# Performance work log

Hardware: AMD Instinct MI355X
Metric: run time of the kernel (lower is better)

The kernel has to match this reference:

```python
import jax, jax.numpy as jnp
import numpy as np

NUM_NODES = 200000
NUM_EDGES = 300000
NUM_QUERIES = 128
NUM_ENTITIES = 50000
N_DIMS = 256
N_DIMS_SM = 64
STATIC_DIM = 128
STATIC_SM = 32
G_IN = 2 * N_DIMS_SM + STATIC_SM + N_DIMS_SM  # 224


def leaky(x):
    return jnp.where(x > 0, x, 0.01 * x)


def setup_inputs() -> dict:
    key = jax.random.key(0)
    ks = jax.random.split(key, 24)
    W = 0.05  # weight scale to keep logits in a sane range
    inp = {
        'memorized_embedding': jax.random.normal(ks[0], (NUM_NODES, N_DIMS), jnp.float32),
        'node_score': jax.random.uniform(ks[1], (NUM_NODES,), jnp.float32),
        'rel_emb': jax.random.normal(ks[2], (NUM_EDGES, N_DIMS), jnp.float32),
        'query_src_ts_emb': jax.random.normal(ks[3], (NUM_QUERIES, STATIC_DIM), jnp.float32),
        'query_rel_emb': jax.random.normal(ks[4], (NUM_QUERIES, N_DIMS), jnp.float32),
        'eg_idx': jax.random.randint(ks[5], (NUM_EDGES,), 0, NUM_QUERIES, jnp.int32),
        'src_idx': jax.random.randint(ks[6], (NUM_EDGES,), 0, NUM_NODES, jnp.int32),
        'dst_idx': jax.random.randint(ks[7], (NUM_EDGES,), 0, NUM_NODES, jnp.int32),
        'entity_idx': jax.random.randint(ks[8], (NUM_NODES,), 0, NUM_ENTITIES, jnp.int32),
        'W_proj': W * jax.random.normal(ks[9], (N_DIMS, N_DIMS_SM), jnp.float32),
        'b_proj': W * jax.random.normal(ks[10], (N_DIMS_SM,), jnp.float32),
        'W_static': W * jax.random.normal(ks[11], (STATIC_DIM, STATIC_SM), jnp.float32),
        'b_static': W * jax.random.normal(ks[12], (STATIC_SM,), jnp.float32),
        'W_bs': W * jax.random.normal(ks[13], (N_DIMS, N_DIMS), jnp.float32),
        'b_bs': W * jax.random.normal(ks[14], (N_DIMS,), jnp.float32),
        'Wl': W * jax.random.normal(ks[15], (G_IN, N_DIMS_SM), jnp.float32),
        'bl': W * jax.random.normal(ks[16], (N_DIMS_SM,), jnp.float32),
        'Wr': W * jax.random.normal(ks[17], (G_IN, N_DIMS_SM), jnp.float32),
        'br': W * jax.random.normal(ks[18], (N_DIMS_SM,), jnp.float32),
        'Wc': W * jax.random.normal(ks[19], (N_DIMS_SM, N_DIMS_SM), jnp.float32),
        'bc': W * jax.random.normal(ks[20], (N_DIMS_SM,), jnp.float32),
    }
    return inp


def reference(memorized_embedding, node_score, rel_emb, query_src_ts_emb, query_rel_emb,
              eg_idx, src_idx, dst_idx, entity_idx,
              W_proj, b_proj, W_static, b_static, W_bs, b_bs,
              Wl, bl, Wr, br, Wc, bc):
    # one attention-flow step: linear_between_steps -> attention scoring (G) ->
    # per-source-node softmax -> attention propagation -> per-entity aggregation
    emb2 = leaky(memorized_embedding @ W_bs + b_bs)        # [N, d]
    # project all node embeddings once (linear commutes with gather)
    proj_all = emb2 @ W_proj + b_proj                       # [N, d_sm]
    hvi = proj_all[src_idx]                                 # [E, d_sm]
    hvj = proj_all[dst_idx]                                 # [E, d_sm]
    rel = rel_emb @ W_proj + b_proj                         # [E, d_sm]
    # context_dim_red
    qs = query_src_ts_emb @ W_static + b_static             # [B, static_sm]
    qr = query_rel_emb @ W_proj + b_proj                    # [B, d_sm]
    qs_e = qs[eg_idx]                                       # [E, static_sm]
    qr_e = qr[eg_idx]                                       # [E, d_sm]
    left = jnp.concatenate([hvi, rel, qs_e, qr_e], axis=-1)   # [E, G_IN]
    right = jnp.concatenate([hvj, rel, qs_e, qr_e], axis=-1)  # [E, G_IN]
    # G: sum(leaky(left W_l) * ((leaky(right W_r)) W_c))
    lh = leaky(left @ Wl + bl)                              # [E, d_sm]
    rh = leaky(right @ Wr + br) @ Wc + bc                   # [E, d_sm]
    logits = jnp.sum(lh * rh, axis=-1)                      # [E]
    # transition probability: softmax over outgoing edges of each source node
    seg_max = jax.ops.segment_max(logits, src_idx, num_segments=NUM_NODES)
    ex = jnp.exp(logits - seg_max[src_idx])
    denom = jax.ops.segment_sum(ex, src_idx, num_segments=NUM_NODES)
    trans = ex / denom[src_idx]
    # propagate node attention along edges (node_score_aggregation='sum')
    new_node_score = jax.ops.segment_sum(trans * node_score[src_idx], dst_idx,
                                         num_segments=NUM_NODES)
    # _aggregate_op_entity: sparse COO matmul == segment_sum over entity groups
    entity_att_score = jax.ops.segment_sum(new_node_score, entity_idx,
                                           num_segments=NUM_ENTITIES)
    return entity_att_score
```

## Files before the change

### kernel.cpp

```cpp
#include <hip/hip_runtime.h>
#include <hip/hip_bf16.h>

#define N_NODES 200000
#define N_EDGES 300000
#define N_Q     128
#define N_ENT   50000
#define D       256
#define DSM     64
#define SDIM    128
#define SSM     32

typedef __attribute__((ext_vector_type(8))) short bf16x8;
typedef __attribute__((ext_vector_type(4))) float f32x4;

__device__ __forceinline__ float leaky(float x){ return x > 0.f ? x : 0.01f*x; }

__device__ __forceinline__ unsigned short f2bf(float f){
  __hip_bfloat16 h = __float2bfloat16(f);
  return *reinterpret_cast<unsigned short*>(&h);
}
__device__ __forceinline__ unsigned pk2bf(float a, float b){
  float2 t; t.x = a; t.y = b;
  __hip_bfloat162 h = __float22bfloat162_rn(t);
  return *reinterpret_cast<unsigned*>(&h);
}
__device__ __forceinline__ float bf2f(unsigned short h){
  return __uint_as_float(((unsigned)h) << 16);
}

__device__ __forceinline__ void dev_pack(const float* __restrict__ src,
                                         unsigned short* __restrict__ dst,
                                         int K, int N, int id, int total){
  if (id >= total) return;
  int lane = id & 63, fb = id >> 6;
  int KB = K >> 5;
  int kb = fb % KB, nb = fb / KB;
  int k0 = kb*32 + ((lane>>4)<<3);
  int n  = nb*16 + (lane & 15);
  #pragma unroll
  for (int i = 0; i < 8; ++i) dst[(size_t)id*8 + i] = f2bf(src[(size_t)(k0+i)*N + n]);
}

__global__ void k_setup1(float* out, float* denom,
                         const float* __restrict__ Wp, const float* __restrict__ Wl,
                         const float* __restrict__ Wr, float* Wnlr, float* Wrlr,
                         const float* __restrict__ bp, float* cv,
                         const float* __restrict__ qsrc, const float* __restrict__ Ws,
                         const float* __restrict__ bs, const float* __restrict__ qrel,
                         float* qs, float* qr,
                         const float* __restrict__ Wbs, unsigned short* Wbs_pk,
                         const float* __restrict__ Wc, unsigned short* Wc_pk){
  int b = blockIdx.x, tid = threadIdx.x;
  if (b < 782){
    int id = b*256 + tid;
    if (id < N_ENT) out[id] = 0.f;
    if (id < N_NODES) denom[id] = 0.f;
  } else if (b < 1038){
    int id = (b-782)*256 + tid;
    int m = id >> 14, rem = id & 16383, k = rem >> 6, c = rem & 63;
    const float* Wsrc = (m & 1) ? Wr : Wl;
    int roff = (m >> 1) * 64;
    float s = 0.f;
    for (int i = 0; i < 64; ++i) s += Wp[k*64+i] * Wsrc[(roff+i)*64 + c];
    float* o = (m >> 1) ? Wrlr : Wnlr;
    o[k*128 + (m&1)*64 + c] = s;
  } else if (b == 1038){
    int m = tid >> 6, c = tid & 63;
    const float* Wsrc = (m & 1) ? Wr : Wl;
    int roff = (m >> 1) * 64;
    float s = 0.f;
    for (int i = 0; i < 64; ++i) s += bp[i] * Wsrc[(roff+i)*64 + c];
    cv[tid] = s;
  } else if (b < 1087){
    int id = (b-1039)*256 + tid;
    if (id < N_Q*SSM){
      int q = id >> 5, i = id & 31;
      float s = bs[i];
      for (int j = 0; j < SDIM; ++j) s += qsrc[q*SDIM+j] * Ws[j*SSM+i];
      qs[id] = s;
    } else {
      int id2 = id - N_Q*SSM;
      int q = id2 >> 6, i = id2 & 63;
      float s = bp[i];
      for (int j = 0; j < D; ++j) s += qrel[q*D+j] * Wp[j*DSM+i];
      qr[id2] = s;
    }
  } else if (b < 1119){
    dev_pack(Wbs, Wbs_pk, 256, 256, (b-1087)*256 + tid, 8192);
  } else {
    dev_pack(Wc, Wc_pk, 64, 64, (b-1119)*256 + tid, 512);
  }
}

__global__ void k_setup2(const float* __restrict__ qs, const float* __restrict__ qr,
                         const float* __restrict__ Wl, const float* __restrict__ bl,
                         const float* __restrict__ Wr, const float* __restrict__ br,
                         unsigned* qctx_p,
                         const float* __restrict__ Wnlr, unsigned short* Wn_pk,
                         const float* __restrict__ Wrlr, unsigned short* Wr_pk){
  int b = blockIdx.x, tid = threadIdx.x;
  if (b < 32){
    int id = b*256 + tid;
    int q = id >> 6, c = id & 63;
    float sl = bl[c], sr = br[c];
    for (int i = 0; i < SSM; ++i){
      float v = qs[q*SSM+i];
      sl += v * Wl[(128+i)*64+c];
      sr += v * Wr[(128+i)*64+c];
    }
    for (int i = 0; i < DSM; ++i){
      float v = qr[q*DSM+i];
      sl += v * Wl[(160+i)*64+c];
      sr += v * Wr[(160+i)*64+c];
    }
    qctx_p[id] = pk2bf(sl, sr);
  } else if (b < 48){
    dev_pack(Wnlr, Wn_pk, 256, 128, (b-32)*256 + tid, 4096);
  } else {
    dev_pack(Wrlr, Wr_pk, 256, 128, (b-48)*256 + tid, 4096);
  }
}

__global__ __launch_bounds__(256) void k_node(const float* __restrict__ A,
    const unsigned short* __restrict__ Wbs_pk, const float* __restrict__ bbs,
    const unsigned short* __restrict__ Wn_pk, const float* __restrict__ cv,
    unsigned short* __restrict__ node_l, unsigned short* __restrict__ node_r){
  __shared__ char smem[32768];
  int tid = threadIdx.x;
  int row0 = blockIdx.x * 64;
  {
    const float4* Ag = (const float4*)(A + (size_t)row0 * 256);
    #pragma unroll
    for (int it = 0; it < 16; ++it){
      int f = tid + 256*it;
      int r = f >> 6, c4 = f & 63;
      float4 v = Ag[f];
      uint2 u;
      u.x = pk2bf(v.x, v.y);
      u.y = pk2bf(v.z, v.w);
      int byte = (r << 9) + (c4 << 3);
      byte ^= (r & 7) << 4;
      *(uint2*)(smem + byte) = u;
    }
  }
  __syncthreads();
  int l = tid & 63, wn = tid >> 6;
  f32x4 acc[4][4];
  #pragma unroll
  for (int mf = 0; mf < 4; ++mf)
    #pragma unroll
    for (int nf = 0; nf < 4; ++nf) acc[mf][nf] = (f32x4){0.f,0.f,0.f,0.f};
  for (int kb = 0; kb < 8; ++kb){
    bf16x8 a[4], b[4];
    #pragma unroll
    for (int mf = 0; mf < 4; ++mf){
      int row = mf*16 + (l & 15);
      int byte = (row << 9) + kb*64 + ((l >> 4) << 4);
      byte ^= (row & 7) << 4;
      a[mf] = *(const bf16x8*)(smem + byte);
    }
    #pragma unroll
    for (int nf = 0; nf < 4; ++nf){
      int nb = wn*4 + nf;
      b[nf] = *(const bf16x8*)(Wbs_pk + ((size_t)(nb*8 + kb)*64 + l)*8);
    }
    #pragma unroll
    for (int mf = 0; mf < 4; ++mf)
      #pragma unroll
      for (int nf = 0; nf < 4; ++nf)
        acc[mf][nf] = __builtin_amdgcn_mfma_f32_16x16x32_bf16(a[mf], b[nf], acc[mf][nf], 0, 0, 0);
  }
  __syncthreads();
  #pragma unroll
  for (int mf = 0; mf < 4; ++mf)
    #pragma unroll
    for (int nf = 0; nf < 4; ++nf){
      int col = wn*64 + nf*16 + (l & 15);
      float bb = bbs[col];
      #pragma unroll
      for (int r = 0; r < 4; ++r){
        int row = mf*16 + ((l >> 4) << 2) + r;
        int byte = (row << 9) + col*2;
        byte ^= (row & 7) << 4;
        *(unsigned short*)(smem + byte) = f2bf(leaky(acc[mf][nf][r] + bb));
      }
    }
  __syncthreads();
  f32x4 acc2[4][2];
  #pragma unroll
  for (int mf = 0; mf < 4; ++mf){ acc2[mf][0] = (f32x4){0.f,0.f,0.f,0.f}; acc2[mf][1] = (f32x4){0.f,0.f,0.f,0.f}; }
  for (int kb = 0; kb < 8; ++kb){
    bf16x8 a[4], b[2];
    #pragma unroll
    for (int mf = 0; mf < 4; ++mf){
      int row = mf*16 + (l & 15);
      int byte = (row << 9) + kb*64 + ((l >> 4) << 4);
      byte ^= (row & 7) << 4;
      a[mf] = *(const bf16x8*)(smem + byte);
    }
    #pragma unroll
    for (int nf = 0; nf < 2; ++nf){
      int nb = wn*2 + nf;
      b[nf] = *(const bf16x8*)(Wn_pk + ((size_t)(nb*8 + kb)*64 + l)*8);
    }
    #pragma unroll
    for (int mf = 0; mf < 4; ++mf)
      #pragma unroll
      for (int nf = 0; nf < 2; ++nf)
        acc2[mf][nf] = __builtin_amdgcn_mfma_f32_16x16x32_bf16(a[mf], b[nf], acc2[mf][nf], 0, 0, 0);
  }
  #pragma unroll
  for (int mf = 0; mf < 4; ++mf)
    #pragma unroll
    for (int nf = 0; nf < 2; ++nf){
      int col = wn*32 + nf*16 + (l & 15);
      float cc = cv[col];
      #pragma unroll
      for (int r = 0; r < 4; ++r){
        int row = mf*16 + ((l >> 4) << 2) + r;
        unsigned short h = f2bf(acc2[mf][nf][r] + cc);
        size_t g = (size_t)(row0 + row);
        if (col < 64) node_l[g*64 + col] = h;
        else          node_r[g*64 + col - 64] = h;
      }
    }
}

__global__ __launch_bounds__(256) void k_edge(const float* __restrict__ relE,
    const unsigned short* __restrict__ Wr_pk, const unsigned short* __restrict__ Wc_pk,
    const float* __restrict__ cv, const float* __restrict__ bc,
    const unsigned short* __restrict__ node_l, const unsigned short* __restrict__ node_r,
    const unsigned* __restrict__ qctx_p,
    const int* __restrict__ src, const int* __restrict__ dst, const int* __restrict__ eg,
    float* __restrict__ exbuf, float* __restrict__ denom){
  __shared__ char smem[32768];
  unsigned short* sRL  = (unsigned short*)smem;
  char*           sLc  = smem + 16384;
  char*           sRin = smem + 24576;
  int tid = threadIdx.x;
  int e0 = blockIdx.x * 64;
  int l = tid & 63, wn = tid >> 6;

  int idxv;
  {
    int j = l & 15;
    int e = e0 + wn*16 + j;
    int ec = e < N_EDGES ? e : N_EDGES-1;
    const int* p = (l < 16) ? src : (l < 32) ? dst : eg;
    idxv = p[ec];
  }
  {
    const float4* Rg = (const float4*)relE;
    #pragma unroll
    for (int it = 0; it < 16; ++it){
      int f = tid + 256*it;
      int r = f >> 6, c4 = f & 63;
      int ge = e0 + r;
      float4 v = make_float4(0.f,0.f,0.f,0.f);
      if (ge < N_EDGES) v = Rg[(size_t)ge*64 + c4];
      uint2 u;
      u.x = pk2bf(v.x, v.y);
      u.y = pk2bf(v.z, v.w);
      int byte = (r << 9) + (c4 << 3);
      byte ^= (r & 7) << 4;
      *(uint2*)(smem + byte) = u;
    }
  }
  __syncthreads();

  f32x4 acc[4][2];
  #pragma unroll
  for (int mf = 0; mf < 4; ++mf){ acc[mf][0] = (f32x4){0.f,0.f,0.f,0.f}; acc[mf][1] = (f32x4){0.f,0.f,0.f,0.f}; }
  for (int kb = 0; kb < 8; ++kb){
    bf16x8 a[4], b[2];
    #pragma unroll
    for (int mf = 0; mf < 4; ++mf){
      int row = mf*16 + (l & 15);
      int byte = (row << 9) + kb*64 + ((l >> 4) << 4);
      byte ^= (row & 7) << 4;
      a[mf] = *(const bf16x8*)(smem + byte);
    }
    #pragma unroll
    for (int nf = 0; nf < 2; ++nf){
      int nb = wn*2 + nf;
      b[nf] = *(const bf16x8*)(Wr_pk + ((size_t)(nb*8 + kb)*64 + l)*8);
    }
    #pragma unroll
    for (int mf = 0; mf < 4; ++mf)
      #pragma unroll
      for (int nf = 0; nf < 2; ++nf)
        acc[mf][nf] = __builtin_amdgcn_mfma_f32_16x16x32_bf16(a[mf], b[nf], acc[mf][nf], 0, 0, 0);
  }
  __syncthreads();
  #pragma unroll
  for (int mf = 0; mf < 4; ++mf)
    #pragma unroll
    for (int nf = 0; nf < 2; ++nf){
      int col = wn*32 + nf*16 + (l & 15);
      float cc = cv[128 + col];
      #pragma unroll
      for (int r = 0; r < 4; ++r){
        int row = mf*16 + ((l >> 4) << 2) + r;
        int byte = (row << 8) + (col << 1);
        byte ^= (row & 12) << 3;
        *(unsigned short*)((char*)sRL + byte) = f2bf(acc[mf][nf][r] + cc);
      }
    }
  __syncthreads();
  #pragma unroll
  for (int j = 0; j < 16; ++j){
    int er = wn*16 + j;
    int e = e0 + er;
    int byteL = (er << 8) + (l << 1);      byteL ^= (er & 12) << 3;
    int byteR = (er << 8) + ((64+l) << 1); byteR ^= (er & 12) << 3;
    int bL = (er << 7) + (l << 1);         bL ^= (er & 12) << 3;
    int bR = (er << 7) + (l << 1);         bR ^= (er & 7) << 4;
    unsigned short lh16 = 0, rr16 = 0;
    if (e < N_EDGES){
      int s  = __shfl(idxv, j);
      int d2 = __shfl(idxv, 16 + j);
      int b  = __shfl(idxv, 32 + j);
      unsigned qv = qctx_p[b*64 + l];
      float lh = leaky(bf2f(node_l[(size_t)s*64 + l]) + bf2f(*(unsigned short*)((char*)sRL + byteL))
                       + bf2f((unsigned short)(qv & 0xFFFFu)));
      float rr = leaky(bf2f(node_r[(size_t)d2*64 + l]) + bf2f(*(unsigned short*)((char*)sRL + byteR))
                       + bf2f((unsigned short)(qv >> 16)));
      lh16 = f2bf(lh); rr16 = f2bf(rr);
    }
    *(unsigned short*)(sLc + bL) = lh16;
    *(unsigned short*)(sRin + bR) = rr16;
  }

  float bcv[4];
  #pragma unroll
  for (int nf = 0; nf < 4; ++nf) bcv[nf] = bc[nf*16 + (l & 15)];
  f32x4 acc2[4];
  #pragma unroll
  for (int nf = 0; nf < 4; ++nf) acc2[nf] = (f32x4){0.f,0.f,0.f,0.f};
  #pragma unroll
  for (int kb = 0; kb < 2; ++kb){
    int row = wn*16 + (l & 15);
    int byte = (row << 7) + kb*64 + ((l >> 4) << 4);
    byte ^= (row & 7) << 4;
    bf16x8 a = *(const bf16x8*)(sRin + byte);
    #pragma unroll
    for (int nf = 0; nf < 4; ++nf){
      bf16x8 bfr = *(const bf16x8*)(Wc_pk + ((size_t)(nf*2 + kb)*64 + l)*8);
      acc2[nf] = __builtin_amdgcn_mfma_f32_16x16x32_bf16(a, bfr, acc2[nf], 0, 0, 0);
    }
  }
  int srcj[4];
  float vr[4];
  #pragma unroll
  for (int r = 0; r < 4; ++r){
    int rowl = ((l >> 4) << 2) + r;
    srcj[r] = __shfl(idxv, rowl);
    int row = wn*16 + rowl;
    float v = 0.f;
    #pragma unroll
    for (int nf = 0; nf < 4; ++nf){
      int col = nf*16 + (l & 15);
      int byte = (row << 7) + (col << 1);
      byte ^= (row & 12) << 3;
      v += (acc2[nf][r] + bcv[nf]) * bf2f(*(unsigned short*)(sLc + byte));
    }
    v += __shfl_xor(v, 1); v += __shfl_xor(v, 2);
    v += __shfl_xor(v, 4); v += __shfl_xor(v, 8);
    vr[r] = v;
  }
  if ((l & 15) == 0){
    #pragma unroll
    for (int r = 0; r < 4; ++r){
      int rowl = ((l >> 4) << 2) + r;
      int e = e0 + wn*16 + rowl;
      if (e < N_EDGES){
        float ex = __expf(vr[r]);
        exbuf[e] = ex;
        atomicAdd(&denom[srcj[r]], ex);
      }
    }
  }
}

__global__ void k_passC(const float* __restrict__ exbuf, const float* __restrict__ denom,
                        const int* __restrict__ src, const int* __restrict__ dst,
                        const float* __restrict__ node_score, const int* __restrict__ ent,
                        float* __restrict__ out){
  int e = blockIdx.x*256 + threadIdx.x;
  if (e >= N_EDGES) return;
  int s = src[e];
  float tr = exbuf[e] / denom[s];
  atomicAdd(&out[ent[dst[e]]], tr * node_score[s]);
}

extern "C" void kernel_launch(void* const* d_in, const int* in_sizes, int n_in,
                              void* d_out, int out_size, void* d_ws, size_t ws_size,
                              hipStream_t stream){
  const float* mem   = (const float*)d_in[0];
  const float* nsc   = (const float*)d_in[1];
  const float* relE  = (const float*)d_in[2];
  const float* qsrc  = (const float*)d_in[3];
  const float* qrel  = (const float*)d_in[4];
  const int*   eg    = (const int*)d_in[5];
  const int*   src   = (const int*)d_in[6];
  const int*   dst   = (const int*)d_in[7];
  const int*   ent   = (const int*)d_in[8];
  const float* Wp    = (const float*)d_in[9];
  const float* bp    = (const float*)d_in[10];
  const float* Ws    = (const float*)d_in[11];
  const float* bs    = (const float*)d_in[12];
  const float* Wbs   = (const float*)d_in[13];
  const float* bbs   = (const float*)d_in[14];
  const float* Wl    = (const float*)d_in[15];
  const float* bl    = (const float*)d_in[16];
  const float* Wr    = (const float*)d_in[17];
  const float* br    = (const float*)d_in[18];
  const float* Wc    = (const float*)d_in[19];
  const float* bc    = (const float*)d_in[20];
  float* out = (float*)d_out;

  char* w = (char*)d_ws;
  auto alloc = [&](size_t bytes)->void*{
    void* p = (void*)w; w += (bytes + 255) & ~(size_t)255; return p;
  };
  float* Wnlr = (float*)alloc(32768*4);
  float* Wrlr = (float*)alloc(32768*4);
  unsigned short* Wbs_pk = (unsigned short*)alloc(65536*2);
  unsigned short* Wn_pk  = (unsigned short*)alloc(32768*2);
  unsigned short* Wr_pk  = (unsigned short*)alloc(32768*2);
  unsigned short* Wc_pk  = (unsigned short*)alloc(4096*2);
  float* cv  = (float*)alloc(256*4);
  float* qs  = (float*)alloc((size_t)N_Q*SSM*4);
  float* qr  = (float*)alloc((size_t)N_Q*DSM*4);
  unsigned* qctx_p = (unsigned*)alloc((size_t)N_Q*DSM*4);
  unsigned short* node_l = (unsigned short*)alloc((size_t)N_NODES*64*2);
  unsigned short* node_r = (unsigned short*)alloc((size_t)N_NODES*64*2);
  float* exbuf  = (float*)alloc((size_t)N_EDGES*4);
  float* denom = (float*)alloc((size_t)N_NODES*4);

  k_setup1<<<1121, 256, 0, stream>>>(out, denom,
                                     Wp, Wl, Wr, Wnlr, Wrlr, bp, cv,
                                     qsrc, Ws, bs, qrel, qs, qr,
                                     Wbs, Wbs_pk, Wc, Wc_pk);
  k_setup2<<<64, 256, 0, stream>>>(qs, qr, Wl, bl, Wr, br, qctx_p,
                                   Wnlr, Wn_pk, Wrlr, Wr_pk);
  k_node<<<N_NODES/64, 256, 0, stream>>>(mem, Wbs_pk, bbs, Wn_pk, cv, node_l, node_r);
  k_edge<<<(N_EDGES+63)/64, 256, 0, stream>>>(relE, Wr_pk, Wc_pk, cv, bc,
                                              node_l, node_r, qctx_p,
                                              src, dst, eg, exbuf, denom);
  k_passC<<<(N_EDGES+255)/256, 256, 0, stream>>>(exbuf, denom, src, dst, nsc, ent, out);
}
```

Baseline: 275.6 us.

## Make k_edge wave-independent: load rel rows directly into MFMA fragments, drop block syncs

Each wavefront now owns its own 16 edges across all 128 output columns. It reads the rel_emb rows from global memory straight into bf16 A fragments instead of staging a 64-row tile in shared memory and splitting columns across waves. This removes the shared-memory staging pass and every __syncthreads, and gives each wave a private LDS slice, so waves can run independently. Launch bounds also request 5 blocks per CU. In exchange each wave loads the full Wr weight set (4x more B-fragment loads per block), and its global reads of rel_emb are strided per row rather than fully coalesced.

```diff
diff --git a/kernel.cpp b/kernel.cpp
--- a/kernel.cpp
+++ b/kernel.cpp
@@ -226,7 +226,7 @@
     }
 }
 
-__global__ __launch_bounds__(256) void k_edge(const float* __restrict__ relE,
+__global__ __launch_bounds__(256, 5) void k_edge(const float* __restrict__ relE,
     const unsigned short* __restrict__ Wr_pk, const unsigned short* __restrict__ Wc_pk,
     const float* __restrict__ cv, const float* __restrict__ bc,
     const unsigned short* __restrict__ node_l, const unsigned short* __restrict__ node_r,
@@ -234,103 +234,76 @@
     const int* __restrict__ src, const int* __restrict__ dst, const int* __restrict__ eg,
     float* __restrict__ exbuf, float* __restrict__ denom){
   __shared__ char smem[32768];
-  unsigned short* sRL  = (unsigned short*)smem;
-  char*           sLc  = smem + 16384;
-  char*           sRin = smem + 24576;
   int tid = threadIdx.x;
-  int e0 = blockIdx.x * 64;
   int l = tid & 63, wn = tid >> 6;
+  char* wbase = smem + wn*8192;
+  char* sRL  = wbase;
+  char* sLc  = wbase + 4096;
+  char* sRin = wbase + 6144;
+  int e0 = blockIdx.x * 64 + wn*16;
 
   int idxv;
   {
     int j = l & 15;
-    int e = e0 + wn*16 + j;
+    int e = e0 + j;
     int ec = e < N_EDGES ? e : N_EDGES-1;
     const int* p = (l < 16) ? src : (l < 32) ? dst : eg;
     idxv = p[ec];
   }
-  {
-    const float4* Rg = (const float4*)relE;
-    #pragma unroll
-    for (int it = 0; it < 16; ++it){
-      int f = tid + 256*it;
-      int r = f >> 6, c4 = f & 63;
-      int ge = e0 + r;
-      float4 v = make_float4(0.f,0.f,0.f,0.f);
-      if (ge < N_EDGES) v = Rg[(size_t)ge*64 + c4];
-      uint2 u;
-      u.x = pk2bf(v.x, v.y);
-      u.y = pk2bf(v.z, v.w);
-      int byte = (r << 9) + (c4 << 3);
-      byte ^= (r & 7) << 4;
-      *(uint2*)(smem + byte) = u;
-    }
-  }
-  __syncthreads();
-
-  f32x4 acc[4][2];
-  #pragma unroll
-  for (int mf = 0; mf < 4; ++mf){ acc[mf][0] = (f32x4){0.f,0.f,0.f,0.f}; acc[mf][1] = (f32x4){0.f,0.f,0.f,0.f}; }
+
+  int arow = e0 + (l & 15);
+  if (arow >= N_EDGES) arow = N_EDGES - 1;
+  const float4* Rg = (const float4*)relE;
+  size_t rbase = (size_t)arow * 64 + ((l >> 4) << 1);
+  f32x4 acc[8];
+  #pragma unroll
+  for (int nb = 0; nb < 8; ++nb) acc[nb] = (f32x4){0.f,0.f,0.f,0.f};
   for (int kb = 0; kb < 8; ++kb){
-    bf16x8 a[4], b[2];
-    #pragma unroll
-    for (int mf = 0; mf < 4; ++mf){
-      int row = mf*16 + (l & 15);
-      int byte = (row << 9) + kb*64 + ((l >> 4) << 4);
-      byte ^= (row & 7) << 4;
-      a[mf] = *(const bf16x8*)(smem + byte);
-    }
-    #pragma unroll
-    for (int nf = 0; nf < 2; ++nf){
-      int nb = wn*2 + nf;
-      b[nf] = *(const bf16x8*)(Wr_pk + ((size_t)(nb*8 + kb)*64 + l)*8);
-    }
-    #pragma unroll
-    for (int mf = 0; mf < 4; ++mf)
-      #pragma unroll
-      for (int nf = 0; nf < 2; ++nf)
-        acc[mf][nf] = __builtin_amdgcn_mfma_f32_16x16x32_bf16(a[mf], b[nf], acc[mf][nf], 0, 0, 0);
-  }
-  __syncthreads();
-  #pragma unroll
-  for (int mf = 0; mf < 4; ++mf)
-    #pragma unroll
-    for (int nf = 0; nf < 2; ++nf){
-      int col = wn*32 + nf*16 + (l & 15);
-      float cc = cv[128 + col];
-      #pragma unroll
-      for (int r = 0; r < 4; ++r){
-        int row = mf*16 + ((l >> 4) << 2) + r;
-        int byte = (row << 8) + (col << 1);
-        byte ^= (row & 12) << 3;
-        *(unsigned short*)((char*)sRL + byte) = f2bf(acc[mf][nf][r] + cc);
-      }
-    }
-  __syncthreads();
+    float4 v0 = Rg[rbase + kb*8];
+    float4 v1 = Rg[rbase + kb*8 + 1];
+    union { bf16x8 v; unsigned u[4]; } au;
+    au.u[0] = pk2bf(v0.x, v0.y); au.u[1] = pk2bf(v0.z, v0.w);
+    au.u[2] = pk2bf(v1.x, v1.y); au.u[3] = pk2bf(v1.z, v1.w);
+    #pragma unroll
+    for (int nb = 0; nb < 8; ++nb){
+      bf16x8 b = *(const bf16x8*)(Wr_pk + ((size_t)(nb*8 + kb)*64 + l)*8);
+      acc[nb] = __builtin_amdgcn_mfma_f32_16x16x32_bf16(au.v, b, acc[nb], 0, 0, 0);
+    }
+  }
+  #pragma unroll
+  for (int nb = 0; nb < 8; ++nb){
+    int col = nb*16 + (l & 15);
+    float cc = cv[128 + col];
+    #pragma unroll
+    for (int r = 0; r < 4; ++r){
+      int row = ((l >> 4) << 2) + r;
+      int byte = (row << 8) + (col << 1);
+      byte ^= (row & 12) << 3;
+      *(unsigned short*)(sRL + byte) = f2bf(acc[nb][r] + cc);
+    }
+  }
   #pragma unroll
   for (int j = 0; j < 16; ++j){
-    int er = wn*16 + j;
-    int e = e0 + er;
-    int byteL = (er << 8) + (l << 1);      byteL ^= (er & 12) << 3;
-    int byteR = (er << 8) + ((64+l) << 1); byteR ^= (er & 12) << 3;
-    int bL = (er << 7) + (l << 1);         bL ^= (er & 12) << 3;
-    int bR = (er << 7) + (l << 1);         bR ^= (er & 7) << 4;
+    int e = e0 + j;
+    int byteL = (j << 8) + (l << 1);        byteL ^= (j & 12) << 3;
+    int byteR = (j << 8) + ((64+l) << 1);   byteR ^= (j & 12) << 3;
+    int bL = (j << 7) + (l << 1);           bL ^= (j & 12) << 3;
+    int bR = (j << 7) + (l << 1);           bR ^= (j & 7) << 4;
     unsigned short lh16 = 0, rr16 = 0;
     if (e < N_EDGES){
       int s  = __shfl(idxv, j);
       int d2 = __shfl(idxv, 16 + j);
       int b  = __shfl(idxv, 32 + j);
       unsigned qv = qctx_p[b*64 + l];
-      float lh = leaky(bf2f(node_l[(size_t)s*64 + l]) + bf2f(*(unsigned short*)((char*)sRL + byteL))
+      float lh = leaky(bf2f(node_l[(size_t)s*64 + l]) + bf2f(*(unsigned short*)(sRL + byteL))
                        + bf2f((unsigned short)(qv & 0xFFFFu)));
-      float rr = leaky(bf2f(node_r[(size_t)d2*64 + l]) + bf2f(*(unsigned short*)((char*)sRL + byteR))
+      float rr = leaky(bf2f(node_r[(size_t)d2*64 + l]) + bf2f(*(unsigned short*)(sRL + byteR))
                        + bf2f((unsigned short)(qv >> 16)));
       lh16 = f2bf(lh); rr16 = f2bf(rr);
     }
     *(unsigned short*)(sLc + bL) = lh16;
     *(unsigned short*)(sRin + bR) = rr16;
   }
-
   float bcv[4];
   #pragma unroll
   for (int nf = 0; nf < 4; ++nf) bcv[nf] = bc[nf*16 + (l & 15)];
@@ -339,7 +312,7 @@
   for (int nf = 0; nf < 4; ++nf) acc2[nf] = (f32x4){0.f,0.f,0.f,0.f};
   #pragma unroll
   for (int kb = 0; kb < 2; ++kb){
-    int row = wn*16 + (l & 15);
+    int row = l & 15;
     int byte = (row << 7) + kb*64 + ((l >> 4) << 4);
     byte ^= (row & 7) << 4;
     bf16x8 a = *(const bf16x8*)(sRin + byte);
@@ -355,13 +328,12 @@
   for (int r = 0; r < 4; ++r){
     int rowl = ((l >> 4) << 2) + r;
     srcj[r] = __shfl(idxv, rowl);
-    int row = wn*16 + rowl;
     float v = 0.f;
     #pragma unroll
     for (int nf = 0; nf < 4; ++nf){
       int col = nf*16 + (l & 15);
-      int byte = (row << 7) + (col << 1);
-      byte ^= (row & 12) << 3;
+      int byte = (rowl << 7) + (col << 1);
+      byte ^= (rowl & 12) << 3;
       v += (acc2[nf][r] + bcv[nf]) * bf2f(*(unsigned short*)(sLc + byte));
     }
     v += __shfl_xor(v, 1); v += __shfl_xor(v, 2);
@@ -372,7 +344,7 @@
     #pragma unroll
     for (int r = 0; r < 4; ++r){
       int rowl = ((l >> 4) << 2) + r;
-      int e = e0 + wn*16 + rowl;
+      int e = e0 + rowl;
       if (e < N_EDGES){
         float ex = __expf(vr[r]);
         exbuf[e] = ex;
```

After: 322.6 us. +17.1%, slower.

## Split edge kernel into relation projection and gather-score kernels

Applied to the files above, without the earlier changes.

Breaks the fused edge kernel into k_rel, which projects rel_emb through Wr and writes packed bf16 L/R pairs to a global buffer, and k_score, which gathers node and relation values into registers up front, then runs the Wc MFMA and softmax-numerator accumulation using per-wave shared memory. The goal is to separate the streaming GEMM from the latency-bound random gathers and to raise occupancy of the gather kernel, with loads issued early to hide latency. In exchange it adds a write and read of roughly 77 MB of intermediate rel_pk data plus an extra launch.

```diff
diff --git a/kernel.cpp b/kernel.cpp
--- a/kernel.cpp
+++ b/kernel.cpp
@@ -226,38 +226,20 @@
     }
 }
 
-__global__ __launch_bounds__(256) void k_edge(const float* __restrict__ relE,
-    const unsigned short* __restrict__ Wr_pk, const unsigned short* __restrict__ Wc_pk,
-    const float* __restrict__ cv, const float* __restrict__ bc,
-    const unsigned short* __restrict__ node_l, const unsigned short* __restrict__ node_r,
-    const unsigned* __restrict__ qctx_p,
-    const int* __restrict__ src, const int* __restrict__ dst, const int* __restrict__ eg,
-    float* __restrict__ exbuf, float* __restrict__ denom){
+__global__ __launch_bounds__(256) void k_rel(const float* __restrict__ relE,
+    const unsigned short* __restrict__ Wr_pk, const float* __restrict__ cv,
+    unsigned* __restrict__ rel_pk){
   __shared__ char smem[32768];
-  unsigned short* sRL  = (unsigned short*)smem;
-  char*           sLc  = smem + 16384;
-  char*           sRin = smem + 24576;
   int tid = threadIdx.x;
-  int e0 = blockIdx.x * 64;
-  int l = tid & 63, wn = tid >> 6;
-
-  int idxv;
-  {
-    int j = l & 15;
-    int e = e0 + wn*16 + j;
-    int ec = e < N_EDGES ? e : N_EDGES-1;
-    const int* p = (l < 16) ? src : (l < 32) ? dst : eg;
-    idxv = p[ec];
-  }
+  int row0 = blockIdx.x * 64;
   {
     const float4* Rg = (const float4*)relE;
     #pragma unroll
     for (int it = 0; it < 16; ++it){
       int f = tid + 256*it;
       int r = f >> 6, c4 = f & 63;
-      int ge = e0 + r;
-      float4 v = make_float4(0.f,0.f,0.f,0.f);
-      if (ge < N_EDGES) v = Rg[(size_t)ge*64 + c4];
+      int ge = row0 + r; if (ge >= N_EDGES) ge = N_EDGES-1;
+      float4 v = Rg[(size_t)ge*64 + c4];
       uint2 u;
       u.x = pk2bf(v.x, v.y);
       u.y = pk2bf(v.z, v.w);
@@ -267,12 +249,12 @@
     }
   }
   __syncthreads();
-
+  int l = tid & 63, wn = tid >> 6;
   f32x4 acc[4][2];
   #pragma unroll
   for (int mf = 0; mf < 4; ++mf){ acc[mf][0] = (f32x4){0.f,0.f,0.f,0.f}; acc[mf][1] = (f32x4){0.f,0.f,0.f,0.f}; }
   for (int kb = 0; kb < 8; ++kb){
-    bf16x8 a[4], b[2];
+    bf16x8 a[4], b0, b1;
     #pragma unroll
     for (int mf = 0; mf < 4; ++mf){
       int row = mf*16 + (l & 15);
@@ -280,57 +262,80 @@
       byte ^= (row & 7) << 4;
       a[mf] = *(const bf16x8*)(smem + byte);
     }
-    #pragma unroll
-    for (int nf = 0; nf < 2; ++nf){
-      int nb = wn*2 + nf;
-      b[nf] = *(const bf16x8*)(Wr_pk + ((size_t)(nb*8 + kb)*64 + l)*8);
-    }
-    #pragma unroll
-    for (int mf = 0; mf < 4; ++mf)
-      #pragma unroll
-      for (int nf = 0; nf < 2; ++nf)
-        acc[mf][nf] = __builtin_amdgcn_mfma_f32_16x16x32_bf16(a[mf], b[nf], acc[mf][nf], 0, 0, 0);
-  }
-  __syncthreads();
+    b0 = *(const bf16x8*)(Wr_pk + ((size_t)(wn*8 + kb)*64 + l)*8);
+    b1 = *(const bf16x8*)(Wr_pk + ((size_t)((4+wn)*8 + kb)*64 + l)*8);
+    #pragma unroll
+    for (int mf = 0; mf < 4; ++mf){
+      acc[mf][0] = __builtin_amdgcn_mfma_f32_16x16x32_bf16(a[mf], b0, acc[mf][0], 0, 0, 0);
+      acc[mf][1] = __builtin_amdgcn_mfma_f32_16x16x32_bf16(a[mf], b1, acc[mf][1], 0, 0, 0);
+    }
+  }
+  int c = wn*16 + (l & 15);
+  float cvL = cv[128 + c], cvR = cv[192 + c];
   #pragma unroll
   for (int mf = 0; mf < 4; ++mf)
     #pragma unroll
-    for (int nf = 0; nf < 2; ++nf){
-      int col = wn*32 + nf*16 + (l & 15);
-      float cc = cv[128 + col];
-      #pragma unroll
-      for (int r = 0; r < 4; ++r){
-        int row = mf*16 + ((l >> 4) << 2) + r;
-        int byte = (row << 8) + (col << 1);
-        byte ^= (row & 12) << 3;
-        *(unsigned short*)((char*)sRL + byte) = f2bf(acc[mf][nf][r] + cc);
-      }
-    }
-  __syncthreads();
+    for (int r = 0; r < 4; ++r){
+      int row = mf*16 + ((l >> 4) << 2) + r;
+      int e = row0 + row;
+      if (e < N_EDGES)
+        rel_pk[(size_t)e*64 + c] = pk2bf(acc[mf][0][r] + cvL, acc[mf][1][r] + cvR);
+    }
+}
+
+__global__ __launch_bounds__(256, 4) void k_score(const unsigned* __restrict__ rel_pk,
+    const unsigned short* __restrict__ Wc_pk, const float* __restrict__ bc,
+    const unsigned short* __restrict__ node_l, const unsigned short* __restrict__ node_r,
+    const unsigned* __restrict__ qctx_p,
+    const int* __restrict__ src, const int* __restrict__ dst, const int* __restrict__ eg,
+    float* __restrict__ exbuf, float* __restrict__ denom){
+  __shared__ char smem[16384];
+  int tid = threadIdx.x;
+  int l = tid & 63, wn = tid >> 6;
+  char* wbase = smem + wn*4096;
+  char* sLc  = wbase;
+  char* sRin = wbase + 2048;
+  int e0 = blockIdx.x * 64 + wn*16;
+
+  int idxv;
+  {
+    int j = l & 15;
+    int e = e0 + j;
+    int ec = e < N_EDGES ? e : N_EDGES-1;
+    const int* p = (l < 16) ? src : (l < 32) ? dst : eg;
+    idxv = p[ec];
+  }
+  unsigned rlrv[16];
+  unsigned short nlv[16], nrv[16];
   #pragma unroll
   for (int j = 0; j < 16; ++j){
-    int er = wn*16 + j;
-    int e = e0 + er;
-    int byteL = (er << 8) + (l << 1);      byteL ^= (er & 12) << 3;
-    int byteR = (er << 8) + ((64+l) << 1); byteR ^= (er & 12) << 3;
-    int bL = (er << 7) + (l << 1);         bL ^= (er & 12) << 3;
-    int bR = (er << 7) + (l << 1);         bR ^= (er & 7) << 4;
+    int e = e0 + j;
+    int ec = e < N_EDGES ? e : N_EDGES-1;
+    rlrv[j] = rel_pk[(size_t)ec*64 + l];
+    int s  = __shfl(idxv, j);
+    int d2 = __shfl(idxv, 16 + j);
+    nlv[j] = node_l[(size_t)s*64 + l];
+    nrv[j] = node_r[(size_t)d2*64 + l];
+  }
+  #pragma unroll
+  for (int j = 0; j < 16; ++j){
+    int e = e0 + j;
+    int bL = (j << 7) + (l << 1);  bL ^= (j & 12) << 3;
+    int bR = (j << 7) + (l << 1);  bR ^= (j & 7) << 4;
     unsigned short lh16 = 0, rr16 = 0;
     if (e < N_EDGES){
-      int s  = __shfl(idxv, j);
-      int d2 = __shfl(idxv, 16 + j);
-      int b  = __shfl(idxv, 32 + j);
+      int b = __shfl(idxv, 32 + j);
       unsigned qv = qctx_p[b*64 + l];
-      float lh = leaky(bf2f(node_l[(size_t)s*64 + l]) + bf2f(*(unsigned short*)((char*)sRL + byteL))
+      unsigned rv = rlrv[j];
+      float lh = leaky(bf2f(nlv[j]) + bf2f((unsigned short)(rv & 0xFFFFu))
                        + bf2f((unsigned short)(qv & 0xFFFFu)));
-      float rr = leaky(bf2f(node_r[(size_t)d2*64 + l]) + bf2f(*(unsigned short*)((char*)sRL + byteR))
+      float rr = leaky(bf2f(nrv[j]) + bf2f((unsigned short)(rv >> 16))
                        + bf2f((unsigned short)(qv >> 16)));
       lh16 = f2bf(lh); rr16 = f2bf(rr);
     }
     *(unsigned short*)(sLc + bL) = lh16;
     *(unsigned short*)(sRin + bR) = rr16;
   }
-
   float bcv[4];
   #pragma unroll
   for (int nf = 0; nf < 4; ++nf) bcv[nf] = bc[nf*16 + (l & 15)];
@@ -339,7 +344,7 @@
   for (int nf = 0; nf < 4; ++nf) acc2[nf] = (f32x4){0.f,0.f,0.f,0.f};
   #pragma unroll
   for (int kb = 0; kb < 2; ++kb){
-    int row = wn*16 + (l & 15);
+    int row = l & 15;
     int byte = (row << 7) + kb*64 + ((l >> 4) << 4);
     byte ^= (row & 7) << 4;
     bf16x8 a = *(const bf16x8*)(sRin + byte);
@@ -355,13 +360,12 @@
   for (int r = 0; r < 4; ++r){
     int rowl = ((l >> 4) << 2) + r;
     srcj[r] = __shfl(idxv, rowl);
-    int row = wn*16 + rowl;
     float v = 0.f;
     #pragma unroll
     for (int nf = 0; nf < 4; ++nf){
       int col = nf*16 + (l & 15);
-      int byte = (row << 7) + (col << 1);
-      byte ^= (row & 12) << 3;
+      int byte = (rowl << 7) + (col << 1);
+      byte ^= (rowl & 12) << 3;
       v += (acc2[nf][r] + bcv[nf]) * bf2f(*(unsigned short*)(sLc + byte));
     }
     v += __shfl_xor(v, 1); v += __shfl_xor(v, 2);
@@ -372,7 +376,7 @@
     #pragma unroll
     for (int r = 0; r < 4; ++r){
       int rowl = ((l >> 4) << 2) + r;
-      int e = e0 + wn*16 + rowl;
+      int e = e0 + rowl;
       if (e < N_EDGES){
         float ex = __expf(vr[r]);
         exbuf[e] = ex;
@@ -435,18 +439,20 @@
   unsigned* qctx_p = (unsigned*)alloc((size_t)N_Q*DSM*4);
   unsigned short* node_l = (unsigned short*)alloc((size_t)N_NODES*64*2);
   unsigned short* node_r = (unsigned short*)alloc((size_t)N_NODES*64*2);
+  unsigned* rel_pk = (unsigned*)alloc((size_t)N_EDGES*64*4);
   float* exbuf  = (float*)alloc((size_t)N_EDGES*4);
   float* denom = (float*)alloc((size_t)N_NODES*4);
 
+  int egrid = (N_EDGES + 63) / 64;
   k_setup1<<<1121, 256, 0, stream>>>(out, denom,
                                      Wp, Wl, Wr, Wnlr, Wrlr, bp, cv,
                                      qsrc, Ws, bs, qrel, qs, qr,
                                      Wbs, Wbs_pk, Wc, Wc_pk);
   k_setup2<<<64, 256, 0, stream>>>(qs, qr, Wl, bl, Wr, br, qctx_p,
                                    Wnlr, Wn_pk, Wrlr, Wr_pk);
+  k_rel<<<egrid, 256, 0, stream>>>(relE, Wr_pk, cv, rel_pk);
   k_node<<<N_NODES/64, 256, 0, stream>>>(mem, Wbs_pk, bbs, Wn_pk, cv, node_l, node_r);
-  k_edge<<<(N_EDGES+63)/64, 256, 0, stream>>>(relE, Wr_pk, Wc_pk, cv, bc,
-                                              node_l, node_r, qctx_p,
-                                              src, dst, eg, exbuf, denom);
+  k_score<<<egrid, 256, 0, stream>>>(rel_pk, Wc_pk, bc, node_l, node_r, qctx_p,
+                                     src, dst, eg, exbuf, denom);
   k_passC<<<(N_EDGES+255)/256, 256, 0, stream>>>(exbuf, denom, src, dst, nsc, ent, out);
 }
```

New measurement: 277.1 us. No clear change (+0.5%).
